# Kernel tuning notes

Hardware: AMD Instinct MI355X
Metric: run time of the kernel (lower is better)

## Reference

```python
import jax, jax.numpy as jnp
import numpy as np

D_MODEL = 1024
N_HEADS = 16
HEAD_DIM = D_MODEL // N_HEADS
FF_DIM = 4096
EPS = 1e-5


def _layer_norm(v, g, b):
    mu = jnp.mean(v, axis=-1, keepdims=True)
    var = jnp.mean(jnp.square(v - mu), axis=-1, keepdims=True)
    return (v - mu) * jax.lax.rsqrt(var + EPS) * g + b


def setup_inputs() -> dict:
    key = jax.random.key(0)
    ks = jax.random.split(key, 16)
    s = 0.02
    x = jax.random.normal(ks[0], (2, 2048, D_MODEL), dtype=jnp.float32)
    Wq = jax.random.normal(ks[1], (D_MODEL, D_MODEL), dtype=jnp.float32) * s
    Wk = jax.random.normal(ks[2], (D_MODEL, D_MODEL), dtype=jnp.float32) * s
    Wv = jax.random.normal(ks[3], (D_MODEL, D_MODEL), dtype=jnp.float32) * s
    Wo = jax.random.normal(ks[4], (D_MODEL, D_MODEL), dtype=jnp.float32) * s
    bq = jnp.zeros((D_MODEL,), jnp.float32)
    bk = jnp.zeros((D_MODEL,), jnp.float32)
    bv = jnp.zeros((D_MODEL,), jnp.float32)
    bo = jnp.zeros((D_MODEL,), jnp.float32)
    # per-head Conv1d(kernel=1) == per-head linear; weights [H, out, in]
    W1 = jax.random.normal(ks[5], (N_HEADS, FF_DIM, HEAD_DIM), dtype=jnp.float32) * s
    b1 = jnp.zeros((N_HEADS, FF_DIM), jnp.float32)
    W2 = jax.random.normal(ks[6], (N_HEADS, HEAD_DIM, FF_DIM), dtype=jnp.float32) * s
    b2 = jnp.zeros((N_HEADS, HEAD_DIM), jnp.float32)
    g1 = jnp.ones((D_MODEL,), jnp.float32)
    be1 = jnp.zeros((D_MODEL,), jnp.float32)
    g2 = jnp.ones((D_MODEL,), jnp.float32)
    be2 = jnp.zeros((D_MODEL,), jnp.float32)
    return {"x": x, "Wq": Wq, "bq": bq, "Wk": Wk, "bk": bk, "Wv": Wv, "bv": bv,
            "Wo": Wo, "bo": bo, "W1": W1, "b1": b1, "W2": W2, "b2": b2,
            "g1": g1, "be1": be1, "g2": g2, "be2": be2}


def reference(x, Wq, bq, Wk, bk, Wv, bv, Wo, bo, W1, b1, W2, b2, g1, be1, g2, be2):
    B, S, D = x.shape
    H, hd = N_HEADS, HEAD_DIM
    # --- multi-head self-attention (standard scaled dot-product) ---
    q = (x @ Wq + bq).reshape(B, S, H, hd)
    k = (x @ Wk + bk).reshape(B, S, H, hd)
    v = (x @ Wv + bv).reshape(B, S, H, hd)
    scores = jnp.einsum('bqhd,bkhd->bhqk', q, k) / jnp.sqrt(jnp.float32(hd))
    attn = jax.nn.softmax(scores, axis=-1)          # [B,H,S,S]
    ctx = jnp.einsum('bhqk,bkhd->bqhd', attn, v).reshape(B, S, D)
    residual = ctx @ Wo + bo
    # dropout is identity in eval mode
    x1 = _layer_norm(x + residual, g1, be1)
    # --- per-head feed-forward (Conv1d kernel=1 per head, batched over heads) ---
    xh = x1.reshape(B, S, H, hd)
    h = jax.nn.relu(jnp.einsum('bshd,hfd->bshf', xh, W1) + b1)   # [B,S,H,FF]
    ff = jnp.einsum('bshf,hdf->bshd', h, W2) + b2                 # [B,S,H,hd]
    y = _layer_norm(x1 + ff.reshape(B, S, D), g2, be2)
    return (y, attn)
```

## Files before the change

kernel.cpp:

```cpp
#include <hip/hip_runtime.h>
#include <cstddef>

#define D_M 1024
#define NH 16
#define HD 64
#define FFD 4096
#define SQ 2048
#define BB 2
#define TOK (BB*SQ)
#define EPS 1e-5f

typedef __attribute__((ext_vector_type(8))) short bf16x8;
typedef __attribute__((ext_vector_type(4))) float f32x4;

__device__ inline unsigned short f32_bf16_rne(float f) {
  unsigned int u = __float_as_uint(f);
  unsigned int r = (u + 0x7fffu + ((u >> 16) & 1u)) >> 16;
  return (unsigned short)r;
}

__device__ inline float wave_sum(float v) {
  #pragma unroll
  for (int m = 32; m >= 1; m >>= 1) v += __shfl_xor(v, m);
  return v;
}

__global__ __launch_bounds__(256)
void convert_bf16_k(const float* __restrict__ src, unsigned short* __restrict__ dst, int n4) {
  int i = blockIdx.x * 256 + threadIdx.x;
  if (i >= n4) return;
  float4 v = ((const float4*)src)[i];
  ushort4 h;
  h.x = f32_bf16_rne(v.x); h.y = f32_bf16_rne(v.y);
  h.z = f32_bf16_rne(v.z); h.w = f32_bf16_rne(v.w);
  ((ushort4*)dst)[i] = h;
}

__global__ __launch_bounds__(256)
void transp4_k(const float* __restrict__ W0, const float* __restrict__ W1_,
               const float* __restrict__ W2_, const float* __restrict__ W3,
               unsigned short* __restrict__ h0, unsigned short* __restrict__ h1,
               unsigned short* __restrict__ h2, unsigned short* __restrict__ h3) {
  const float* W; unsigned short* hT;
  switch (blockIdx.z) {
    case 0: W = W0; hT = h0; break;
    case 1: W = W1_; hT = h1; break;
    case 2: W = W2_; hT = h2; break;
    default: W = W3; hT = h3; break;
  }
  __shared__ float tile[64][65];
  const int bn = blockIdx.x * 64;
  const int bk = blockIdx.y * 64;
  const int t = threadIdx.x;
  #pragma unroll
  for (int i = 0; i < 4; ++i) {
    int r = (t >> 4) + i * 16, c = (t & 15) * 4;
    float4 v = *(const float4*)&W[(size_t)(bk + r) * D_M + bn + c];
    tile[r][c] = v.x; tile[r][c + 1] = v.y; tile[r][c + 2] = v.z; tile[r][c + 3] = v.w;
  }
  __syncthreads();
  #pragma unroll
  for (int i = 0; i < 4; ++i) {
    int n = (t >> 4) + i * 16, k = (t & 15) * 4;
    ushort4 h;
    h.x = f32_bf16_rne(tile[k][n]);     h.y = f32_bf16_rne(tile[k + 1][n]);
    h.z = f32_bf16_rne(tile[k + 2][n]); h.w = f32_bf16_rne(tile[k + 3][n]);
    *(ushort4*)&hT[(size_t)(bn + n) * D_M + bk + k] = h;
  }
}

__global__ __launch_bounds__(256)
void qkv_gemm_k(const unsigned short* __restrict__ xh_g,
                const unsigned short* __restrict__ Bqh, const unsigned short* __restrict__ Bkh,
                const unsigned short* __restrict__ Bvh,
                const float* __restrict__ bq, const float* __restrict__ bk, const float* __restrict__ bv,
                unsigned short* __restrict__ qh, unsigned short* __restrict__ kh,
                unsigned short* __restrict__ vth) {
  constexpr int LDK = 40;
  __shared__ unsigned short Ah[64 * LDK];
  __shared__ unsigned short Bh[3][128 * LDK];
  const int tid = threadIdx.x;
  const int wave = tid >> 6, lane = tid & 63;
  const int wm = (wave >> 1) * 32, wn = (wave & 1) * 64;
  const int bn = blockIdx.x * 128, bm = blockIdx.y * 64;
  const int K = D_M;

  f32x4 acc[3][2][4] = {};
  const int sr = tid >> 2, sk = (tid & 3) * 8;
  const int l15 = lane & 15, k8 = (lane >> 4) * 8;

  const unsigned short* Bhp[3] = {Bqh, Bkh, Bvh};

  for (int k0 = 0; k0 < K; k0 += 32) {
    *(uint4*)&Ah[sr * LDK + sk] = *(const uint4*)&xh_g[(size_t)(bm + sr) * K + k0 + sk];
    #pragma unroll
    for (int s = 0; s < 3; ++s) {
      #pragma unroll
      for (int c = 0; c < 2; ++c) {
        int r = sr + c * 64;
        *(uint4*)&Bh[s][r * LDK + sk] = *(const uint4*)&Bhp[s][(size_t)(bn + r) * K + k0 + sk];
      }
    }
    __syncthreads();
    bf16x8 af[2];
    #pragma unroll
    for (int m = 0; m < 2; ++m)
      af[m] = *(bf16x8*)&Ah[(wm + m * 16 + l15) * LDK + k8];
    #pragma unroll
    for (int s = 0; s < 3; ++s) {
      #pragma unroll
      for (int n = 0; n < 4; ++n) {
        bf16x8 b0 = *(bf16x8*)&Bh[s][(wn + n * 16 + l15) * LDK + k8];
        #pragma unroll
        for (int m = 0; m < 2; ++m) {
          if (s == 2) {
            acc[s][m][n] = __builtin_amdgcn_mfma_f32_16x16x32_bf16(af[m], b0, acc[s][m][n], 0, 0, 0);
          } else {
            acc[s][m][n] = __builtin_amdgcn_mfma_f32_16x16x32_bf16(b0, af[m], acc[s][m][n], 0, 0, 0);
          }
        }
      }
    }
    __syncthreads();
  }
  const int kq4 = (lane >> 4) * 4;
  #pragma unroll
  for (int s = 0; s < 2; ++s) {
    const float* bias = (s == 0) ? bq : bk;
    unsigned short* oh = (s == 0) ? qh : kh;
    #pragma unroll
    for (int n = 0; n < 4; ++n) {
      int colb = bn + wn + n * 16 + kq4;
      float4 bv4 = *(const float4*)&bias[colb];
      #pragma unroll
      for (int m = 0; m < 2; ++m) {
        int tok = bm + wm + m * 16 + l15;
        ushort4 h;
        h.x = f32_bf16_rne(acc[s][m][n][0] + bv4.x);
        h.y = f32_bf16_rne(acc[s][m][n][1] + bv4.y);
        h.z = f32_bf16_rne(acc[s][m][n][2] + bv4.z);
        h.w = f32_bf16_rne(acc[s][m][n][3] + bv4.w);
        *(ushort4*)&oh[(size_t)tok * D_M + colb] = h;
      }
    }
  }
  #pragma unroll
  for (int n = 0; n < 4; ++n) {
    int col = bn + wn + n * 16 + l15;
    float bvv = bv[col];
    #pragma unroll
    for (int m = 0; m < 2; ++m) {
      int row0 = bm + wm + m * 16 + kq4;
      ushort4 hv;
      hv.x = f32_bf16_rne(acc[2][m][n][0] + bvv); hv.y = f32_bf16_rne(acc[2][m][n][1] + bvv);
      hv.z = f32_bf16_rne(acc[2][m][n][2] + bvv); hv.w = f32_bf16_rne(acc[2][m][n][3] + bvv);
      size_t idx = (((size_t)(row0 >> 11) * NH + (col >> 6)) * HD + (col & 63)) * SQ + (row0 & 2047);
      *(ushort4*)&vth[idx] = hv;
    }
  }
}

__global__ __launch_bounds__(256)
void proj_gemm_k(const unsigned short* __restrict__ Ah_g,
                 const unsigned short* __restrict__ Bh_g,
                 const float* __restrict__ bias, float* __restrict__ C,
                 int M, int N, int K) {
  constexpr int LDK = 40;
  __shared__ unsigned short Ah[64 * LDK];
  __shared__ unsigned short Bh[128 * LDK];
  const int tid = threadIdx.x;
  const int wave = tid >> 6, lane = tid & 63;
  const int wm = (wave >> 1) * 32, wn = (wave & 1) * 64;
  const int bn = blockIdx.x * 128, bm = blockIdx.y * 64;

  f32x4 acc[2][4] = {};
  const int sr = tid >> 2, sk = (tid & 3) * 8;
  const int l15 = lane & 15, k8 = (lane >> 4) * 8;

  for (int k0 = 0; k0 < K; k0 += 32) {
    *(uint4*)&Ah[sr * LDK + sk] = *(const uint4*)&Ah_g[(size_t)(bm + sr) * K + k0 + sk];
    #pragma unroll
    for (int c = 0; c < 2; ++c) {
      int r = sr + c * 64;
      *(uint4*)&Bh[r * LDK + sk] = *(const uint4*)&Bh_g[(size_t)(bn + r) * K + k0 + sk];
    }
    __syncthreads();
    bf16x8 af[2], bfr[4];
    #pragma unroll
    for (int m = 0; m < 2; ++m)
      af[m] = *(bf16x8*)&Ah[(wm + m * 16 + l15) * LDK + k8];
    #pragma unroll
    for (int n = 0; n < 4; ++n)
      bfr[n] = *(bf16x8*)&Bh[(wn + n * 16 + l15) * LDK + k8];
    #pragma unroll
    for (int m = 0; m < 2; ++m)
      #pragma unroll
      for (int n = 0; n < 4; ++n)
        acc[m][n] = __builtin_amdgcn_mfma_f32_16x16x32_bf16(bfr[n], af[m], acc[m][n], 0, 0, 0);
    __syncthreads();
  }
  const int kq4 = (lane >> 4) * 4;
  #pragma unroll
  for (int n = 0; n < 4; ++n) {
    int colb = bn + wn + n * 16 + kq4;
    float4 bv4 = *(const float4*)&bias[colb];
    #pragma unroll
    for (int m = 0; m < 2; ++m) {
      int tok = bm + wm + m * 16 + l15;
      float4 v = {acc[m][n][0] + bv4.x, acc[m][n][1] + bv4.y,
                  acc[m][n][2] + bv4.z, acc[m][n][3] + bv4.w};
      *(float4*)&C[(size_t)tok * N + colb] = v;
    }
  }
}

__global__ __launch_bounds__(256)
void fused_attn_k(const unsigned short* __restrict__ qh,
                  const unsigned short* __restrict__ kh,
                  const unsigned short* __restrict__ vth,
                  float* __restrict__ attn,
                  unsigned short* __restrict__ ctxh) {
  constexpr int LDK = 72;
  constexpr int NT = SQ / 64;
  __shared__ unsigned short Kth[2][64 * LDK], Vts[2][64 * LDK];
  __shared__ unsigned short Ph[128 * LDK];
  const int tid = threadIdx.x, wave = tid >> 6, lane = tid & 63;
  const int l15 = lane & 15, kq = lane >> 4;
  const int bh = blockIdx.x, b = bh >> 4, h = bh & 15;
  const int q0 = blockIdx.y * 128;

  bf16x8 qfh[2][2];
  #pragma unroll
  for (int qi = 0; qi < 2; ++qi) {
    const size_t qoff = (size_t)(b * SQ + q0 + wave * 32 + qi * 16 + l15) * D_M + h * HD + kq * 8;
    qfh[qi][0] = *(const bf16x8*)&qh[qoff];  qfh[qi][1] = *(const bf16x8*)&qh[qoff + 32];
  }

  const size_t kbase = (size_t)(b * SQ) * D_M + h * HD;
  const size_t vbase = (size_t)bh * HD * SQ;
  const int srow = tid >> 2, sc = (tid & 3) * 16;

  float lsum[2] = {0.f, 0.f};
  {
    const unsigned short* src = &kh[kbase + (size_t)srow * D_M + sc];
    *(uint4*)&Kth[0][srow * LDK + sc] = *(const uint4*)src;
    *(uint4*)&Kth[0][srow * LDK + sc + 8] = *(const uint4*)(src + 8);
  }
  __syncthreads();
  for (int t = 0; t < NT; ++t) {
    const int cur = t & 1;
    const bool pf = (t + 1 < NT);
    uint4 r0, r1;
    if (pf) {
      const unsigned short* src = &kh[kbase + (size_t)((t + 1) * 64 + srow) * D_M + sc];
      r0 = *(const uint4*)src;
      r1 = *(const uint4*)(src + 8);
    }
    #pragma unroll
    for (int n = 0; n < 4; ++n) {
      bf16x8 kb0 = *(bf16x8*)&Kth[cur][(n * 16 + l15) * LDK + kq * 8];
      bf16x8 kb1 = *(bf16x8*)&Kth[cur][(n * 16 + l15) * LDK + 32 + kq * 8];
      #pragma unroll
      for (int qi = 0; qi < 2; ++qi) {
        f32x4 s = {};
        s = __builtin_amdgcn_mfma_f32_16x16x32_bf16(kb0, qfh[qi][0], s, 0, 0, 0);
        s = __builtin_amdgcn_mfma_f32_16x16x32_bf16(kb1, qfh[qi][1], s, 0, 0, 0);
        #pragma unroll
        for (int r = 0; r < 4; ++r) lsum[qi] += __expf(s[r] * 0.125f);
      }
    }
    if (pf) {
      *(uint4*)&Kth[cur ^ 1][srow * LDK + sc] = r0;
      *(uint4*)&Kth[cur ^ 1][srow * LDK + sc + 8] = r1;
    }
    __syncthreads();
  }
  float invl[2];
  #pragma unroll
  for (int qi = 0; qi < 2; ++qi) {
    float l = lsum[qi];
    l += __shfl_xor(l, 16);
    l += __shfl_xor(l, 32);
    invl[qi] = 1.0f / l;
  }

  f32x4 cacc[2][4] = {};
  {
    const unsigned short* srch = &kh[kbase + (size_t)srow * D_M + sc];
    const unsigned short* srcv = &vth[vbase + (size_t)srow * SQ + sc];
    *(uint4*)&Kth[0][srow * LDK + sc] = *(const uint4*)srch;
    *(uint4*)&Kth[0][srow * LDK + sc + 8] = *(const uint4*)(srch + 8);
    *(uint4*)&Vts[0][srow * LDK + sc] = *(const uint4*)srcv;
    *(uint4*)&Vts[0][srow * LDK + sc + 8] = *(const uint4*)(srcv + 8);
  }
  __syncthreads();
  for (int t = 0; t < NT; ++t) {
    const int cur = t & 1;
    const int k0 = t * 64;
    const bool pf = (t + 1 < NT);
    uint4 rk0, rk1, rv0, rv1;
    if (pf) {
      const unsigned short* srch = &kh[kbase + (size_t)(k0 + 64 + srow) * D_M + sc];
      const unsigned short* srcv = &vth[vbase + (size_t)srow * SQ + k0 + 64 + sc];
      rk0 = *(const uint4*)srch; rk1 = *(const uint4*)(srch + 8);
      rv0 = *(const uint4*)srcv; rv1 = *(const uint4*)(srcv + 8);
    }
    #pragma unroll
    for (int n = 0; n < 4; ++n) {
      bf16x8 kb0 = *(bf16x8*)&Kth[cur][(n * 16 + l15) * LDK + kq * 8];
      bf16x8 kb1 = *(bf16x8*)&Kth[cur][(n * 16 + l15) * LDK + 32 + kq * 8];
      #pragma unroll
      for (int qi = 0; qi < 2; ++qi) {
        f32x4 s = {};
        s = __builtin_amdgcn_mfma_f32_16x16x32_bf16(kb0, qfh[qi][0], s, 0, 0, 0);
        s = __builtin_amdgcn_mfma_f32_16x16x32_bf16(kb1, qfh[qi][1], s, 0, 0, 0);
        float4 pv;
        pv.x = __expf(s[0] * 0.125f) * invl[qi];
        pv.y = __expf(s[1] * 0.125f) * invl[qi];
        pv.z = __expf(s[2] * 0.125f) * invl[qi];
        pv.w = __expf(s[3] * 0.125f) * invl[qi];
        const int qrow = wave * 32 + qi * 16 + l15;
        *(float4*)&attn[((size_t)bh * SQ + q0 + qrow) * SQ + k0 + n * 16 + kq * 4] = pv;
        ushort4 p4;
        p4.x = f32_bf16_rne(pv.x); p4.y = f32_bf16_rne(pv.y);
        p4.z = f32_bf16_rne(pv.z); p4.w = f32_bf16_rne(pv.w);
        *(ushort4*)&Ph[qrow * LDK + n * 16 + kq * 4] = p4;
      }
    }
    #pragma unroll
    for (int qi = 0; qi < 2; ++qi) {
      bf16x8 pa0 = *(bf16x8*)&Ph[(wave * 32 + qi * 16 + l15) * LDK + kq * 8];
      bf16x8 pa1 = *(bf16x8*)&Ph[(wave * 32 + qi * 16 + l15) * LDK + 32 + kq * 8];
      #pragma unroll
      for (int n = 0; n < 4; ++n) {
        bf16x8 vb0 = *(bf16x8*)&Vts[cur][(n * 16 + l15) * LDK + kq * 8];
        bf16x8 vb1 = *(bf16x8*)&Vts[cur][(n * 16 + l15) * LDK + 32 + kq * 8];
        cacc[qi][n] = __builtin_amdgcn_mfma_f32_16x16x32_bf16(vb0, pa0, cacc[qi][n], 0, 0, 0);
        cacc[qi][n] = __builtin_amdgcn_mfma_f32_16x16x32_bf16(vb1, pa1, cacc[qi][n], 0, 0, 0);
      }
    }
    if (pf) {
      *(uint4*)&Kth[cur ^ 1][srow * LDK + sc] = rk0;
      *(uint4*)&Kth[cur ^ 1][srow * LDK + sc + 8] = rk1;
      *(uint4*)&Vts[cur ^ 1][srow * LDK + sc] = rv0;
      *(uint4*)&Vts[cur ^ 1][srow * LDK + sc + 8] = rv1;
    }
    __syncthreads();
  }
  #pragma unroll
  for (int qi = 0; qi < 2; ++qi)
    #pragma unroll
    for (int n = 0; n < 4; ++n) {
      ushort4 hh;
      hh.x = f32_bf16_rne(cacc[qi][n][0]); hh.y = f32_bf16_rne(cacc[qi][n][1]);
      hh.z = f32_bf16_rne(cacc[qi][n][2]); hh.w = f32_bf16_rne(cacc[qi][n][3]);
      size_t off = (size_t)(b * SQ + q0 + wave * 32 + qi * 16 + l15) * D_M + h * HD + n * 16 + kq * 4;
      *(ushort4*)&ctxh[off] = hh;
    }
}

__global__ __launch_bounds__(256)
void ff_bf16_k(const unsigned short* __restrict__ x1h,
               const unsigned short* __restrict__ W1h_, const float* __restrict__ b1,
               const unsigned short* __restrict__ W2h_, const float* __restrict__ b2,
               float* __restrict__ out) {
  constexpr int LDW = 72;
  constexpr int LDH = 40;
  __shared__ unsigned short W1sh[2][32 * LDW];
  __shared__ unsigned short W2sh[2][64 * LDH];
  __shared__ unsigned short Hh[128 * LDH];

  const int tid = threadIdx.x;
  const int wave = tid >> 6, lane = tid & 63;
  const int wm = wave >> 1, wf = wave & 1, wd = wave & 1;
  const int h = blockIdx.x;
  const int m0 = blockIdx.y * 128;
  const int l15 = lane & 15, kq = lane >> 4;

  const size_t w1base = (size_t)h * FFD * HD;
  const size_t w2base = (size_t)h * HD * FFD;
  const int r1 = tid >> 3, k1 = (tid & 7) * 8;
  const int r2 = tid >> 2, f2 = (tid & 3) * 8;

  bf16x8 xf[4][2];
  #pragma unroll
  for (int m = 0; m < 4; ++m)
    #pragma unroll
    for (int ks = 0; ks < 2; ++ks) {
      size_t gof = (size_t)(m0 + wm * 64 + m * 16 + l15) * D_M + h * HD + ks * 32 + kq * 8;
      xf[m][ks] = *(const bf16x8*)&x1h[gof];
    }

  {
    *(uint4*)&W1sh[0][r1 * LDW + k1] = *(const uint4*)&W1h_[w1base + (size_t)r1 * HD + k1];
    *(uint4*)&W2sh[0][r2 * LDH + f2] = *(const uint4*)&W2h_[w2base + (size_t)r2 * FFD + f2];
  }
  __syncthreads();

  f32x4 ffacc[4][2] = {};

  for (int ch = 0; ch < FFD / 32; ++ch) {
    const int buf = ch & 1;
    const bool pf = (ch + 1 < FFD / 32);
    uint4 w1h_r, w2h_r;
    if (pf) {
      const int f0n = (ch + 1) * 32;
      w1h_r = *(const uint4*)&W1h_[w1base + (size_t)(f0n + r1) * HD + k1];
      w2h_r = *(const uint4*)&W2h_[w2base + (size_t)r2 * FFD + f0n + f2];
    }
    f32x4 hacc[4] = {};
    #pragma unroll
    for (int ks = 0; ks < 2; ++ks) {
      bf16x8 w1h = *(bf16x8*)&W1sh[buf][(wf * 16 + l15) * LDW + ks * 32 + kq * 8];
      #pragma unroll
      for (int m = 0; m < 4; ++m)
        hacc[m] = __builtin_amdgcn_mfma_f32_16x16x32_bf16(w1h, xf[m][ks], hacc[m], 0, 0, 0);
    }
    {
      const int fb = wf * 16 + kq * 4;
      float4 b1v = *(const float4*)&b1[(size_t)h * FFD + ch * 32 + fb];
      const float bb[4] = {b1v.x, b1v.y, b1v.z, b1v.w};
      #pragma unroll
      for (int m = 0; m < 4; ++m) {
        int tok = wm * 64 + m * 16 + l15;
        ushort4 hh;
        hh.x = f32_bf16_rne(fmaxf(hacc[m][0] + bb[0], 0.0f));
        hh.y = f32_bf16_rne(fmaxf(hacc[m][1] + bb[1], 0.0f));
        hh.z = f32_bf16_rne(fmaxf(hacc[m][2] + bb[2], 0.0f));
        hh.w = f32_bf16_rne(fmaxf(hacc[m][3] + bb[3], 0.0f));
        *(ushort4*)&Hh[tok * LDH + fb] = hh;
      }
    }
    __syncthreads();
    bf16x8 hfr[4];
    #pragma unroll
    for (int m = 0; m < 4; ++m)
      hfr[m] = *(bf16x8*)&Hh[(wm * 64 + m * 16 + l15) * LDH + kq * 8];
    #pragma unroll
    for (int n = 0; n < 2; ++n) {
      bf16x8 w2h = *(bf16x8*)&W2sh[buf][(wd * 32 + n * 16 + l15) * LDH + kq * 8];
      #pragma unroll
      for (int m = 0; m < 4; ++m)
        ffacc[m][n] = __builtin_amdgcn_mfma_f32_16x16x32_bf16(w2h, hfr[m], ffacc[m][n], 0, 0, 0);
    }
    if (pf) {
      *(uint4*)&W1sh[buf ^ 1][r1 * LDW + k1] = w1h_r;
      *(uint4*)&W2sh[buf ^ 1][r2 * LDH + f2] = w2h_r;
    }
    __syncthreads();
  }
  #pragma unroll
  for (int n = 0; n < 2; ++n) {
    int db = wd * 32 + n * 16 + kq * 4;
    float4 b2v = *(const float4*)&b2[(size_t)h * HD + db];
    #pragma unroll
    for (int m = 0; m < 4; ++m) {
      int tok = m0 + wm * 64 + m * 16 + l15;
      float4 v = {ffacc[m][n][0] + b2v.x, ffacc[m][n][1] + b2v.y,
                  ffacc[m][n][2] + b2v.z, ffacc[m][n][3] + b2v.w};
      *(float4*)&out[(size_t)tok * D_M + h * HD + db] = v;
    }
  }
}

template<int BF16OUT>
__global__ __launch_bounds__(256)
void add_ln_kernel(const float* __restrict__ a, const float* __restrict__ r,
                   const float* __restrict__ g, const float* __restrict__ be,
                   float* __restrict__ out, unsigned short* __restrict__ oh) {
  const size_t row = blockIdx.x;
  const int tid = threadIdx.x;
  __shared__ float red1[4];
  __shared__ float red2[4];
  float4 va = ((const float4*)(a + row * D_M))[tid];
  float4 vr = ((const float4*)(r + row * D_M))[tid];
  float v0 = va.x + vr.x, v1 = va.y + vr.y, v2 = va.z + vr.z, v3 = va.w + vr.w;
  float s = v0 + v1 + v2 + v3;
  float sq = v0 * v0 + v1 * v1 + v2 * v2 + v3 * v3;
  s = wave_sum(s);
  sq = wave_sum(sq);
  if ((tid & 63) == 0) { red1[tid >> 6] = s; red2[tid >> 6] = sq; }
  __syncthreads();
  s = red1[0] + red1[1] + red1[2] + red1[3];
  sq = red2[0] + red2[1] + red2[2] + red2[3];
  const float mu = s * (1.0f / D_M);
  const float var = sq * (1.0f / D_M) - mu * mu;
  float x = var + EPS;
  float rs = rsqrtf(x);
  rs = rs * (1.5f - 0.5f * x * rs * rs);
  float4 gg = ((const float4*)g)[tid];
  float4 bb = ((const float4*)be)[tid];
  float4 o = {(v0 - mu) * rs * gg.x + bb.x, (v1 - mu) * rs * gg.y + bb.y,
              (v2 - mu) * rs * gg.z + bb.z, (v3 - mu) * rs * gg.w + bb.w};
  ((float4*)(out + row * D_M))[tid] = o;
  if (BF16OUT) {
    ushort4 h;
    h.x = f32_bf16_rne(o.x); h.y = f32_bf16_rne(o.y);
    h.z = f32_bf16_rne(o.z); h.w = f32_bf16_rne(o.w);
    ((ushort4*)(oh + row * D_M))[tid] = h;
  }
}

extern "C" void kernel_launch(void* const* d_in, const int* in_sizes, int n_in,
                              void* d_out, int out_size, void* d_ws, size_t ws_size,
                              hipStream_t stream) {
  const float* x   = (const float*)d_in[0];
  const float* Wq  = (const float*)d_in[1];
  const float* bq  = (const float*)d_in[2];
  const float* Wk  = (const float*)d_in[3];
  const float* bk  = (const float*)d_in[4];
  const float* Wv  = (const float*)d_in[5];
  const float* bv  = (const float*)d_in[6];
  const float* Wo  = (const float*)d_in[7];
  const float* bo  = (const float*)d_in[8];
  const float* W1  = (const float*)d_in[9];
  const float* b1  = (const float*)d_in[10];
  const float* W2  = (const float*)d_in[11];
  const float* b2  = (const float*)d_in[12];
  const float* g1  = (const float*)d_in[13];
  const float* be1 = (const float*)d_in[14];
  const float* g2  = (const float*)d_in[15];
  const float* be2 = (const float*)d_in[16];

  float* y_out = (float*)d_out;
  float* attn  = (float*)d_out + (size_t)TOK * D_M;

  char* p = (char*)d_ws;
  const size_t MB = 1024 * 1024;
  unsigned short* WqT = (unsigned short*)(p + 0 * MB);
  unsigned short* WkT = (unsigned short*)(p + 2 * MB);
  unsigned short* WvT = (unsigned short*)(p + 4 * MB);
  unsigned short* WoT = (unsigned short*)(p + 6 * MB);
  unsigned short* xh  = (unsigned short*)(p + 8 * MB);
  unsigned short* qh  = (unsigned short*)(p + 16 * MB);
  unsigned short* kh  = (unsigned short*)(p + 24 * MB);
  unsigned short* vth = (unsigned short*)(p + 32 * MB);
  unsigned short* ctxh = (unsigned short*)(p + 40 * MB);
  float* resid = (float*)(p + 48 * MB);
  float* x1b   = (float*)(p + 64 * MB);
  unsigned short* x1c_h = (unsigned short*)(p + 8 * MB);
  unsigned short* W1c_h = (unsigned short*)(p + 16 * MB);
  unsigned short* W2c_h = (unsigned short*)(p + 24 * MB);
  float* ffb = (float*)(p + 32 * MB);

  const dim3 blk(256);
  const int n4_act = TOK * D_M / 4;

  transp4_k<<<dim3(16, 16, 4), blk, 0, stream>>>(Wq, Wk, Wv, Wo, WqT, WkT, WvT, WoT);
  convert_bf16_k<<<dim3(n4_act / 256), blk, 0, stream>>>(x, xh, n4_act);

  qkv_gemm_k<<<dim3(D_M / 128, TOK / 64), blk, 0, stream>>>(
      xh, WqT, WkT, WvT, bq, bk, bv, qh, kh, vth);

  fused_attn_k<<<dim3(BB * NH, SQ / 128), blk, 0, stream>>>(qh, kh, vth, attn, ctxh);

  proj_gemm_k<<<dim3(D_M / 128, TOK / 64), blk, 0, stream>>>(
      ctxh, WoT, bo, resid, TOK, D_M, D_M);
  add_ln_kernel<1><<<dim3(TOK), blk, 0, stream>>>(x, resid, g1, be1, x1b, x1c_h);

  convert_bf16_k<<<dim3(n4_act / 256), blk, 0, stream>>>(W1, W1c_h, n4_act);
  convert_bf16_k<<<dim3(n4_act / 256), blk, 0, stream>>>(W2, W2c_h, n4_act);
  ff_bf16_k<<<dim3(NH, TOK / 128), blk, 0, stream>>>(x1c_h, W1c_h, b1, W2c_h, b2, ffb);
  add_ln_kernel<0><<<dim3(TOK), blk, 0, stream>>>(x1b, ffb, g2, be2, y_out, nullptr);
}
```

Before: 477.1 us.

## Give each FF wave private token rows to drop a barrier; merge weight conversions

The per-head feed-forward kernel now assigns each wave 32 whole tokens and all 32 FF columns of the chunk, instead of a 2x2 split over tokens and FF columns. Each wave therefore reads back only the hidden activations it wrote itself, so the mid-chunk __syncthreads between the ReLU store and the second GEMM is removed. In exchange, each wave reads more W1/W2 fragments from shared memory per chunk. Separately, the two W1/W2 bf16 conversion launches are merged into one grid with two y-slices to save a kernel launch.

New measurement: 521.9 us. 9.4% more time.

```diff
diff --git a/kernel.cpp b/kernel.cpp
--- a/kernel.cpp
+++ b/kernel.cpp
@@ -27,6 +27,20 @@
 
 __global__ __launch_bounds__(256)
 void convert_bf16_k(const float* __restrict__ src, unsigned short* __restrict__ dst, int n4) {
+  int i = blockIdx.x * 256 + threadIdx.x;
+  if (i >= n4) return;
+  float4 v = ((const float4*)src)[i];
+  ushort4 h;
+  h.x = f32_bf16_rne(v.x); h.y = f32_bf16_rne(v.y);
+  h.z = f32_bf16_rne(v.z); h.w = f32_bf16_rne(v.w);
+  ((ushort4*)dst)[i] = h;
+}
+
+__global__ __launch_bounds__(256)
+void convert2_bf16_k(const float* __restrict__ s0, unsigned short* __restrict__ d0,
+                     const float* __restrict__ s1, unsigned short* __restrict__ d1, int n4) {
+  const float* src = blockIdx.y ? s1 : s0;
+  unsigned short* dst = blockIdx.y ? d1 : d0;
   int i = blockIdx.x * 256 + threadIdx.x;
   if (i >= n4) return;
   float4 v = ((const float4*)src)[i];
@@ -372,7 +386,6 @@
 
   const int tid = threadIdx.x;
   const int wave = tid >> 6, lane = tid & 63;
-  const int wm = wave >> 1, wf = wave & 1, wd = wave & 1;
   const int h = blockIdx.x;
   const int m0 = blockIdx.y * 128;
   const int l15 = lane & 15, kq = lane >> 4;
@@ -382,12 +395,12 @@
   const int r1 = tid >> 3, k1 = (tid & 7) * 8;
   const int r2 = tid >> 2, f2 = (tid & 3) * 8;
 
-  bf16x8 xf[4][2];
-  #pragma unroll
-  for (int m = 0; m < 4; ++m)
+  bf16x8 xf[2][2];
+  #pragma unroll
+  for (int m = 0; m < 2; ++m)
     #pragma unroll
     for (int ks = 0; ks < 2; ++ks) {
-      size_t gof = (size_t)(m0 + wm * 64 + m * 16 + l15) * D_M + h * HD + ks * 32 + kq * 8;
+      size_t gof = (size_t)(m0 + wave * 32 + m * 16 + l15) * D_M + h * HD + ks * 32 + kq * 8;
       xf[m][ks] = *(const bf16x8*)&x1h[gof];
     }
 
@@ -397,7 +410,7 @@
   }
   __syncthreads();
 
-  f32x4 ffacc[4][2] = {};
+  f32x4 ffacc[2][4] = {};
 
   for (int ch = 0; ch < FFD / 32; ++ch) {
     const int buf = ch & 1;
@@ -408,40 +421,42 @@
       w1h_r = *(const uint4*)&W1h_[w1base + (size_t)(f0n + r1) * HD + k1];
       w2h_r = *(const uint4*)&W2h_[w2base + (size_t)r2 * FFD + f0n + f2];
     }
-    f32x4 hacc[4] = {};
+    f32x4 hacc[2][2] = {};
     #pragma unroll
     for (int ks = 0; ks < 2; ++ks) {
-      bf16x8 w1h = *(bf16x8*)&W1sh[buf][(wf * 16 + l15) * LDW + ks * 32 + kq * 8];
-      #pragma unroll
-      for (int m = 0; m < 4; ++m)
-        hacc[m] = __builtin_amdgcn_mfma_f32_16x16x32_bf16(w1h, xf[m][ks], hacc[m], 0, 0, 0);
-    }
-    {
-      const int fb = wf * 16 + kq * 4;
+      #pragma unroll
+      for (int nf = 0; nf < 2; ++nf) {
+        bf16x8 w1f = *(bf16x8*)&W1sh[buf][(nf * 16 + l15) * LDW + ks * 32 + kq * 8];
+        #pragma unroll
+        for (int m = 0; m < 2; ++m)
+          hacc[nf][m] = __builtin_amdgcn_mfma_f32_16x16x32_bf16(w1f, xf[m][ks], hacc[nf][m], 0, 0, 0);
+      }
+    }
+    #pragma unroll
+    for (int nf = 0; nf < 2; ++nf) {
+      const int fb = nf * 16 + kq * 4;
       float4 b1v = *(const float4*)&b1[(size_t)h * FFD + ch * 32 + fb];
-      const float bb[4] = {b1v.x, b1v.y, b1v.z, b1v.w};
-      #pragma unroll
-      for (int m = 0; m < 4; ++m) {
-        int tok = wm * 64 + m * 16 + l15;
+      #pragma unroll
+      for (int m = 0; m < 2; ++m) {
+        int tok = wave * 32 + m * 16 + l15;
         ushort4 hh;
-        hh.x = f32_bf16_rne(fmaxf(hacc[m][0] + bb[0], 0.0f));
-        hh.y = f32_bf16_rne(fmaxf(hacc[m][1] + bb[1], 0.0f));
-        hh.z = f32_bf16_rne(fmaxf(hacc[m][2] + bb[2], 0.0f));
-        hh.w = f32_bf16_rne(fmaxf(hacc[m][3] + bb[3], 0.0f));
+        hh.x = f32_bf16_rne(fmaxf(hacc[nf][m][0] + b1v.x, 0.0f));
+        hh.y = f32_bf16_rne(fmaxf(hacc[nf][m][1] + b1v.y, 0.0f));
+        hh.z = f32_bf16_rne(fmaxf(hacc[nf][m][2] + b1v.z, 0.0f));
+        hh.w = f32_bf16_rne(fmaxf(hacc[nf][m][3] + b1v.w, 0.0f));
         *(ushort4*)&Hh[tok * LDH + fb] = hh;
       }
     }
-    __syncthreads();
-    bf16x8 hfr[4];
-    #pragma unroll
-    for (int m = 0; m < 4; ++m)
-      hfr[m] = *(bf16x8*)&Hh[(wm * 64 + m * 16 + l15) * LDH + kq * 8];
-    #pragma unroll
-    for (int n = 0; n < 2; ++n) {
-      bf16x8 w2h = *(bf16x8*)&W2sh[buf][(wd * 32 + n * 16 + l15) * LDH + kq * 8];
-      #pragma unroll
-      for (int m = 0; m < 4; ++m)
-        ffacc[m][n] = __builtin_amdgcn_mfma_f32_16x16x32_bf16(w2h, hfr[m], ffacc[m][n], 0, 0, 0);
+    bf16x8 hfr[2];
+    #pragma unroll
+    for (int m = 0; m < 2; ++m)
+      hfr[m] = *(bf16x8*)&Hh[(wave * 32 + m * 16 + l15) * LDH + kq * 8];
+    #pragma unroll
+    for (int n = 0; n < 4; ++n) {
+      bf16x8 w2f = *(bf16x8*)&W2sh[buf][(n * 16 + l15) * LDH + kq * 8];
+      #pragma unroll
+      for (int m = 0; m < 2; ++m)
+        ffacc[m][n] = __builtin_amdgcn_mfma_f32_16x16x32_bf16(w2f, hfr[m], ffacc[m][n], 0, 0, 0);
     }
     if (pf) {
       *(uint4*)&W1sh[buf ^ 1][r1 * LDW + k1] = w1h_r;
@@ -450,12 +465,12 @@
     __syncthreads();
   }
   #pragma unroll
-  for (int n = 0; n < 2; ++n) {
-    int db = wd * 32 + n * 16 + kq * 4;
+  for (int n = 0; n < 4; ++n) {
+    int db = n * 16 + kq * 4;
     float4 b2v = *(const float4*)&b2[(size_t)h * HD + db];
     #pragma unroll
-    for (int m = 0; m < 4; ++m) {
-      int tok = m0 + wm * 64 + m * 16 + l15;
+    for (int m = 0; m < 2; ++m) {
+      int tok = m0 + wave * 32 + m * 16 + l15;
       float4 v = {ffacc[m][n][0] + b2v.x, ffacc[m][n][1] + b2v.y,
                   ffacc[m][n][2] + b2v.z, ffacc[m][n][3] + b2v.w};
       *(float4*)&out[(size_t)tok * D_M + h * HD + db] = v;
@@ -558,8 +573,7 @@
       ctxh, WoT, bo, resid, TOK, D_M, D_M);
   add_ln_kernel<1><<<dim3(TOK), blk, 0, stream>>>(x, resid, g1, be1, x1b, x1c_h);
 
-  convert_bf16_k<<<dim3(n4_act / 256), blk, 0, stream>>>(W1, W1c_h, n4_act);
-  convert_bf16_k<<<dim3(n4_act / 256), blk, 0, stream>>>(W2, W2c_h, n4_act);
+  convert2_bf16_k<<<dim3(n4_act / 256, 2), blk, 0, stream>>>(W1, W1c_h, W2, W2c_h, n4_act);
   ff_bf16_k<<<dim3(NH, TOK / 128), blk, 0, stream>>>(x1c_h, W1c_h, b1, W2c_h, b2, ffb);
   add_ln_kernel<0><<<dim3(TOK), blk, 0, stream>>>(x1b, ffb, g2, be2, y_out, nullptr);
 }
```
